# Kernel optimization log

Hardware: AMD Instinct MI355X
Metric: run time of the kernel (lower is better)

Reference implementation:

```python
import jax, jax.numpy as jnp
import numpy as np

S = 7  # output_size
B, C, HF, WF = 8, 256, 160, 160
N = 128
IMG = 640


def setup_inputs() -> dict:
    key = jax.random.key(0)
    k1, k2, k3, k4 = jax.random.split(key, 4)
    feature_map = jax.random.normal(k1, (B, C, HF, WF), jnp.float32)
    # boxes in image-pixel coordinates (the module divides by image_size itself)
    pts = jax.random.uniform(k2, (B, N, 2, 2), jnp.float32, 0.0, float(IMG))
    lo = jnp.min(pts, axis=2)  # (x1, y1)
    hi = jnp.max(pts, axis=2)  # (x2, y2)
    bboxes = jnp.concatenate([lo, hi], axis=-1)  # [B, N, 4]
    proj_w = jax.random.normal(k3, (C, C), jnp.float32) * (1.0 / np.sqrt(C))
    proj_b = jax.random.normal(k4, (C,), jnp.float32) * 0.01
    return {"feature_map": feature_map, "bboxes": bboxes,
            "proj_w": proj_w, "proj_b": proj_b,
            "image_h": IMG, "image_w": IMG}


def _forward(feature_map, bboxes, proj_w, proj_b, image_h, image_w):
    Bb, Cc, Hf, Wf = feature_map.shape
    # 1x1 conv projection
    f = jnp.einsum('bchw,oc->bohw', feature_map, proj_w) + proj_b[None, :, None, None]
    # scale boxes from image coords to feature coords, then integer clip (as in torch code)
    sx = float(Wf) / float(image_w)
    sy = float(Hf) / float(image_h)
    x1 = jnp.clip(jnp.floor(bboxes[..., 0] * sx).astype(jnp.int32), 0, Wf - 1)
    y1 = jnp.clip(jnp.floor(bboxes[..., 1] * sy).astype(jnp.int32), 0, Hf - 1)
    x2 = jnp.clip(jnp.floor(bboxes[..., 2] * sx).astype(jnp.int32), x1 + 1, Wf)
    y2 = jnp.clip(jnp.floor(bboxes[..., 3] * sy).astype(jnp.int32), y1 + 1, Hf)
    Lx = x2 - x1  # [B, N], >= 1 by construction
    Ly = y2 - y1
    i = jnp.arange(S, dtype=jnp.int32)
    # adaptive_avg_pool2d bin edges: start=floor(i*L/S), end=ceil((i+1)*L/S)
    rs = y1[..., None] + (i * Ly[..., None]) // S            # [B, N, S]
    re = y1[..., None] + ((i + 1) * Ly[..., None] + S - 1) // S
    cs = x1[..., None] + (i * Lx[..., None]) // S
    ce = x1[..., None] + ((i + 1) * Lx[..., None] + S - 1) // S
    # summed-area table (zero-padded): I[b,c,y,x] = sum of f[b,c,:y,:x]
    I = jnp.cumsum(jnp.cumsum(f, axis=2), axis=3)
    I = jnp.pad(I, ((0, 0), (0, 0), (1, 0), (1, 0)))

    def per_batch(Ib, rs_b, re_b, cs_b, ce_b):
        # Ib: [C, Hf+1, Wf+1]; index arrays: [N, S]
        tl = Ib[:, rs_b[:, :, None], cs_b[:, None, :]]
        tr = Ib[:, rs_b[:, :, None], ce_b[:, None, :]]
        bl = Ib[:, re_b[:, :, None], cs_b[:, None, :]]
        br = Ib[:, re_b[:, :, None], ce_b[:, None, :]]
        return br - tr - bl + tl  # [C, N, S, S]

    sums = jax.vmap(per_batch)(I, rs, re, cs, ce)  # [B, C, N, S, S]
    counts = ((re - rs)[..., :, None] * (ce - cs)[..., None, :]).astype(f.dtype)  # [B, N, S, S]
    region_features = jnp.transpose(sums, (0, 2, 1, 3, 4)) / counts[:, :, None, :, :]
    # area in raw bbox units, as in the original code
    area_ratios = (bboxes[..., 2] - bboxes[..., 0]) * (bboxes[..., 3] - bboxes[..., 1])
    return region_features, area_ratios


def reference(feature_map, bboxes, proj_w, proj_b, image_h, image_w):
    return _forward(feature_map, bboxes, proj_w, proj_b, image_h, image_w)
```

## Files before the change

kernel.cpp:

```cpp
#include <hip/hip_runtime.h>
#include <hip/hip_bf16.h>

#define BB 8
#define NN 128
#define CC 256
#define HFD 160
#define WFD 160
#define SS 7
#define REGION_OUT_ELEMS (8*128*256*49)

typedef short short8 __attribute__((ext_vector_type(8)));
typedef float f32x4  __attribute__((ext_vector_type(4)));

__global__ __launch_bounds__(256) void k0_convert_w(const float* __restrict__ W,
                                                    __hip_bfloat16* __restrict__ Wb) {
    int o = blockIdx.x;
    int c = threadIdx.x;
    Wb[o * CC + c] = __float2bfloat16(W[o * CC + c]);
}

__global__ __launch_bounds__(256) void k1_rowsum_transpose(const float* __restrict__ fm,
                                                           float* __restrict__ R) {
    int bid = blockIdx.x;
    int cq  = bid & 3;
    int bh  = bid >> 2;
    int h   = bh % HFD;
    int b   = bh / HFD;
    int c0  = cq * 64;
    int t   = threadIdx.x;

    __shared__ float tile[64][161];
    __shared__ float segsum[64][5];

    #pragma unroll
    for (int it = 0; it < 10; ++it) {
        int vid = it * 256 + t;
        int c_l = vid / 40;
        int wq  = vid - c_l * 40;
        f32x4 v = __builtin_nontemporal_load(
            (const f32x4*)(fm + (((size_t)(b * CC + c0 + c_l)) * HFD + h) * WFD + wq * 4));
        tile[c_l][wq * 4 + 0] = v.x;
        tile[c_l][wq * 4 + 1] = v.y;
        tile[c_l][wq * 4 + 2] = v.z;
        tile[c_l][wq * 4 + 3] = v.w;
    }
    __syncthreads();

    int seg = t >> 6;
    int row = t & 63;
    {
        float s = 0.f;
        int w0 = seg * 40;
        #pragma unroll 8
        for (int k = 0; k < 40; ++k) {
            s += tile[row][w0 + k];
            tile[row][w0 + k] = s;
        }
        segsum[row][seg] = s;
    }
    __syncthreads();
    if (t < 64) {
        float a0 = segsum[t][0];
        float a1 = a0 + segsum[t][1];
        float a2 = a1 + segsum[t][2];
        segsum[t][1] = a0;
        segsum[t][2] = a1;
        segsum[t][3] = a2;
    }
    __syncthreads();
    if (seg > 0) {
        float off = segsum[row][seg];
        int w0 = seg * 40;
        #pragma unroll 8
        for (int k = 0; k < 40; ++k) tile[row][w0 + k] += off;
    }
    __syncthreads();

    size_t obase = (((size_t)b * HFD + h) * WFD) * CC + c0;
    #pragma unroll
    for (int it = 0; it < 10; ++it) {
        int vid = it * 256 + t;
        int w   = vid >> 4;
        int cg  = vid & 15;
        float4 o;
        o.x = tile[cg * 4 + 0][w];
        o.y = tile[cg * 4 + 1][w];
        o.z = tile[cg * 4 + 2][w];
        o.w = tile[cg * 4 + 3][w];
        *(float4*)(R + obase + (size_t)w * CC + cg * 4) = o;
    }
}

__global__ __launch_bounds__(256) void k2_colsum(float* __restrict__ I) {
    int w = blockIdx.x % WFD;
    int b = blockIdx.x / WFD;
    int c = threadIdx.x;
    float* p = I + (((size_t)b * HFD) * WFD + w) * CC + c;
    const size_t stride = (size_t)WFD * CC;
    float s = 0.f;
    #pragma unroll 16
    for (int h = 0; h < HFD; ++h) {
        float v = p[(size_t)h * stride];
        s += v;
        p[(size_t)h * stride] = s;
    }
}

#define PB_STRIDE 264

__global__ __launch_bounds__(512) void k3_gather_gemm(
        const float* __restrict__ I, const __hip_bfloat16* __restrict__ Wb,
        const float* __restrict__ bias, const float* __restrict__ bboxes,
        const int* __restrict__ ih_p, const int* __restrict__ iw_p,
        float* __restrict__ out) {
    int bid = blockIdx.x;
    int bn  = ((bid & 7) << 7) | (bid >> 3);
    int b   = bn >> 7;
    int t   = threadIdx.x;
    const int lane = t & 63;
    const int wv   = t >> 6;

    __shared__ __align__(16) __hip_bfloat16 Pb[64 * PB_STRIDE];
    float* stage = (float*)Pb;

    float bx1 = bboxes[bn * 4 + 0];
    float by1 = bboxes[bn * 4 + 1];
    float bx2 = bboxes[bn * 4 + 2];
    float by2 = bboxes[bn * 4 + 3];
    float sx = (float)WFD / (float)iw_p[0];
    float sy = (float)HFD / (float)ih_p[0];

    int x1 = min(max((int)floorf(bx1 * sx), 0), WFD - 1);
    int y1 = min(max((int)floorf(by1 * sy), 0), HFD - 1);
    int x2 = min(max((int)floorf(bx2 * sx), x1 + 1), WFD);
    int y2 = min(max((int)floorf(by2 * sy), y1 + 1), HFD);
    int Lx = x2 - x1, Ly = y2 - y1;

    {
        const float* Ibl = I + (size_t)b * HFD * WFD * CC + 4 * lane;
        unsigned short* pbs = (unsigned short*)Pb;

#define GATHER_CELL(cellv)                                                       \
        {                                                                        \
            int cell = (cellv);                                                  \
            int i_ = cell / SS, j_ = cell % SS;                                  \
            int rs_ = y1 + (i_ * Ly) / SS;                                       \
            int re_ = y1 + ((i_ + 1) * Ly + SS - 1) / SS;                        \
            int cs_ = x1 + (j_ * Lx) / SS;                                       \
            int ce_ = x1 + ((j_ + 1) * Lx + SS - 1) / SS;                        \
            int r1 = re_ - 1;                                                    \
            int r0 = max(rs_ - 1, 0);                                            \
            int c1 = ce_ - 1;                                                    \
            int c0 = max(cs_ - 1, 0);                                            \
            float rm = (rs_ > 0) ? 1.f : 0.f;                                    \
            float cm = (cs_ > 0) ? 1.f : 0.f;                                    \
            f32x4 br = *(const f32x4*)(Ibl + ((size_t)(r1 * WFD + c1)) * CC);    \
            f32x4 tr = *(const f32x4*)(Ibl + ((size_t)(r0 * WFD + c1)) * CC);    \
            f32x4 bl = *(const f32x4*)(Ibl + ((size_t)(r1 * WFD + c0)) * CC);    \
            f32x4 tl = *(const f32x4*)(Ibl + ((size_t)(r0 * WFD + c0)) * CC);    \
            f32x4 s = (br - tr * rm) - (bl - tl * rm) * cm;                      \
            float inv = 1.f / ((float)(re_ - rs_) * (float)(ce_ - cs_));         \
            ushort4 pk;                                                          \
            {                                                                    \
                __hip_bfloat16 h0 = __float2bfloat16(s.x * inv);                 \
                __hip_bfloat16 h1 = __float2bfloat16(s.y * inv);                 \
                __hip_bfloat16 h2 = __float2bfloat16(s.z * inv);                 \
                __hip_bfloat16 h3 = __float2bfloat16(s.w * inv);                 \
                pk.x = *(unsigned short*)&h0;                                    \
                pk.y = *(unsigned short*)&h1;                                    \
                pk.z = *(unsigned short*)&h2;                                    \
                pk.w = *(unsigned short*)&h3;                                    \
            }                                                                    \
            *(ushort4*)(pbs + cell * PB_STRIDE + 4 * lane) = pk;                 \
        }

        #pragma unroll
        for (int k = 0; k < 6; ++k) GATHER_CELL(wv * 6 + k);
        if (wv == 0) GATHER_CELL(48);
#undef GATHER_CELL
    }
    __syncthreads();

    const int ln   = lane & 15;
    const int quad = lane >> 4;
    const int ob0  = wv * 32;

    f32x4 z = {0.f, 0.f, 0.f, 0.f};
    f32x4 acc[2][4];
    #pragma unroll
    for (int mt = 0; mt < 2; ++mt)
        #pragma unroll
        for (int nt = 0; nt < 4; ++nt) acc[mt][nt] = z;

    {
        const short* A = (const short*)Wb;
        #pragma unroll
        for (int k0 = 0; k0 < CC; k0 += 32) {
            short8 a[2], bf[4];
            #pragma unroll
            for (int mt = 0; mt < 2; ++mt)
                a[mt] = *(const short8*)(A + (ob0 + mt * 16 + ln) * CC + k0 + quad * 8);
            #pragma unroll
            for (int nt = 0; nt < 4; ++nt)
                bf[nt] = *(const short8*)((const short*)Pb + (nt * 16 + ln) * PB_STRIDE + k0 + quad * 8);
            #pragma unroll
            for (int mt = 0; mt < 2; ++mt)
                #pragma unroll
                for (int nt = 0; nt < 4; ++nt)
                    acc[mt][nt] = __builtin_amdgcn_mfma_f32_16x16x32_bf16(a[mt], bf[nt], acc[mt][nt], 0, 0, 0);
        }
    }

    size_t obase = (size_t)bn * CC * 49;
    #pragma unroll
    for (int half = 0; half < 2; ++half) {
        __syncthreads();
        if ((wv >> 2) == half) {
            int ob0l = (wv & 3) * 32;
            #pragma unroll
            for (int mt = 0; mt < 2; ++mt) {
                f32x4 bv = *(const f32x4*)(bias + ob0 + mt * 16 + quad * 4);
                #pragma unroll
                for (int nt = 0; nt < 4; ++nt) {
                    int cell = nt * 16 + ln;
                    if (cell < 49) {
                        #pragma unroll
                        for (int reg = 0; reg < 4; ++reg) {
                            int ol = ob0l + mt * 16 + quad * 4 + reg;
                            stage[ol * 49 + cell] = acc[mt][nt][reg] + bv[reg];
                        }
                    }
                }
            }
        }
        __syncthreads();
        const f32x4* sv = (const f32x4*)stage;
        float* gbase = out + obase + (size_t)half * (128 * 49);
        for (int i = t; i < (128 * 49) / 4; i += 512) {
            __builtin_nontemporal_store(sv[i], (f32x4*)(gbase + 4 * i));
        }
    }

    if (t == 0) {
        __builtin_nontemporal_store((bx2 - bx1) * (by2 - by1), &out[REGION_OUT_ELEMS + bn]);
    }
}

extern "C" void kernel_launch(void* const* d_in, const int* in_sizes, int n_in,
                              void* d_out, int out_size, void* d_ws, size_t ws_size,
                              hipStream_t stream) {
    const float* fm     = (const float*)d_in[0];
    const float* bboxes = (const float*)d_in[1];
    const float* W      = (const float*)d_in[2];
    const float* bias   = (const float*)d_in[3];
    const int*   ih     = (const int*)d_in[4];
    const int*   iw     = (const int*)d_in[5];
    float* out = (float*)d_out;

    __hip_bfloat16* Wb = (__hip_bfloat16*)d_ws;
    float* I = (float*)((char*)d_ws + (size_t)CC * CC * 2 + 256);
    I = (float*)(((uintptr_t)I + 1023) & ~(uintptr_t)1023);

    k0_convert_w<<<CC, 256, 0, stream>>>(W, Wb);
    k1_rowsum_transpose<<<BB * HFD * 4, 256, 0, stream>>>(fm, I);
    k2_colsum<<<BB * WFD, 256, 0, stream>>>(I);
    k3_gather_gemm<<<BB * NN, 512, 0, stream>>>(I, Wb, bias, bboxes, ih, iw, out);
}
```

Measured before the change: 411.0 us.

## Fuse column prefix into row-scan kernel with per-block offsets

The row-scan kernel now processes 8 consecutive rows per block and keeps a running column sum in registers, so it writes a blockwise-inclusive integral image in one pass. The separate full read-modify-write column-sum pass over the 210MB table is replaced by a small kernel that only computes per-block row offsets. The gather kernel adds these offsets at lookup time, which doubles its gather loads (eight instead of four per cell). It also gets a launch_bounds occupancy hint. The block grid shrinks to 640 blocks, which may reduce parallelism during the scan.

```diff
diff --git a/kernel.cpp b/kernel.cpp
--- a/kernel.cpp
+++ b/kernel.cpp
@@ -7,6 +7,8 @@
 #define HFD 160
 #define WFD 160
 #define SS 7
+#define HB 8
+#define NHB (HFD / HB)
 #define REGION_OUT_ELEMS (8*128*256*49)
 
 typedef short short8 __attribute__((ext_vector_type(8)));
@@ -19,97 +21,106 @@
     Wb[o * CC + c] = __float2bfloat16(W[o * CC + c]);
 }
 
-__global__ __launch_bounds__(256) void k1_rowsum_transpose(const float* __restrict__ fm,
-                                                           float* __restrict__ R) {
+__global__ __launch_bounds__(256) void k1_rowscan_block(const float* __restrict__ fm,
+                                                        float* __restrict__ Ip) {
     int bid = blockIdx.x;
-    int cq  = bid & 3;
-    int bh  = bid >> 2;
-    int h   = bh % HFD;
-    int b   = bh / HFD;
+    int hb  = bid % NHB;
+    int cq  = (bid / NHB) & 3;
+    int b   = bid / (NHB * 4);
     int c0  = cq * 64;
     int t   = threadIdx.x;
 
     __shared__ float tile[64][161];
     __shared__ float segsum[64][5];
 
-    #pragma unroll
-    for (int it = 0; it < 10; ++it) {
-        int vid = it * 256 + t;
-        int c_l = vid / 40;
-        int wq  = vid - c_l * 40;
-        f32x4 v = __builtin_nontemporal_load(
-            (const f32x4*)(fm + (((size_t)(b * CC + c0 + c_l)) * HFD + h) * WFD + wq * 4));
-        tile[c_l][wq * 4 + 0] = v.x;
-        tile[c_l][wq * 4 + 1] = v.y;
-        tile[c_l][wq * 4 + 2] = v.z;
-        tile[c_l][wq * 4 + 3] = v.w;
-    }
-    __syncthreads();
-
     int seg = t >> 6;
     int row = t & 63;
-    {
-        float s = 0.f;
-        int w0 = seg * 40;
-        #pragma unroll 8
-        for (int k = 0; k < 40; ++k) {
-            s += tile[row][w0 + k];
-            tile[row][w0 + k] = s;
-        }
-        segsum[row][seg] = s;
-    }
-    __syncthreads();
-    if (t < 64) {
-        float a0 = segsum[t][0];
-        float a1 = a0 + segsum[t][1];
-        float a2 = a1 + segsum[t][2];
-        segsum[t][1] = a0;
-        segsum[t][2] = a1;
-        segsum[t][3] = a2;
-    }
-    __syncthreads();
-    if (seg > 0) {
-        float off = segsum[row][seg];
-        int w0 = seg * 40;
-        #pragma unroll 8
-        for (int k = 0; k < 40; ++k) tile[row][w0 + k] += off;
-    }
-    __syncthreads();
-
-    size_t obase = (((size_t)b * HFD + h) * WFD) * CC + c0;
-    #pragma unroll
-    for (int it = 0; it < 10; ++it) {
-        int vid = it * 256 + t;
-        int w   = vid >> 4;
-        int cg  = vid & 15;
-        float4 o;
-        o.x = tile[cg * 4 + 0][w];
-        o.y = tile[cg * 4 + 1][w];
-        o.z = tile[cg * 4 + 2][w];
-        o.w = tile[cg * 4 + 3][w];
-        *(float4*)(R + obase + (size_t)w * CC + cg * 4) = o;
-    }
-}
-
-__global__ __launch_bounds__(256) void k2_colsum(float* __restrict__ I) {
+
+    f32x4 csum[10];
+    #pragma unroll
+    for (int it = 0; it < 10; ++it) csum[it] = (f32x4){0.f, 0.f, 0.f, 0.f};
+
+    for (int hh = 0; hh < HB; ++hh) {
+        int h = hb * HB + hh;
+        __syncthreads();
+
+        #pragma unroll
+        for (int it = 0; it < 10; ++it) {
+            int vid = it * 256 + t;
+            int c_l = vid / 40;
+            int wq  = vid - c_l * 40;
+            f32x4 v = __builtin_nontemporal_load(
+                (const f32x4*)(fm + (((size_t)(b * CC + c0 + c_l)) * HFD + h) * WFD + wq * 4));
+            tile[c_l][wq * 4 + 0] = v.x;
+            tile[c_l][wq * 4 + 1] = v.y;
+            tile[c_l][wq * 4 + 2] = v.z;
+            tile[c_l][wq * 4 + 3] = v.w;
+        }
+        __syncthreads();
+
+        {
+            float s = 0.f;
+            int w0 = seg * 40;
+            #pragma unroll 8
+            for (int k = 0; k < 40; ++k) {
+                s += tile[row][w0 + k];
+                tile[row][w0 + k] = s;
+            }
+            segsum[row][seg] = s;
+        }
+        __syncthreads();
+        if (t < 64) {
+            float a0 = segsum[t][0];
+            float a1 = a0 + segsum[t][1];
+            float a2 = a1 + segsum[t][2];
+            segsum[t][1] = a0;
+            segsum[t][2] = a1;
+            segsum[t][3] = a2;
+        }
+        __syncthreads();
+        if (seg > 0) {
+            float off = segsum[row][seg];
+            int w0 = seg * 40;
+            #pragma unroll 8
+            for (int k = 0; k < 40; ++k) tile[row][w0 + k] += off;
+        }
+        __syncthreads();
+
+        size_t obase = (((size_t)b * HFD + h) * WFD) * CC + c0;
+        #pragma unroll
+        for (int it = 0; it < 10; ++it) {
+            int vid = it * 256 + t;
+            int w   = vid >> 4;
+            int cg  = vid & 15;
+            f32x4 cur;
+            cur.x = tile[cg * 4 + 0][w];
+            cur.y = tile[cg * 4 + 1][w];
+            cur.z = tile[cg * 4 + 2][w];
+            cur.w = tile[cg * 4 + 3][w];
+            csum[it] += cur;
+            *(f32x4*)(Ip + obase + (size_t)w * CC + cg * 4) = csum[it];
+        }
+    }
+}
+
+__global__ __launch_bounds__(256) void k2_offsets(const float* __restrict__ Ip,
+                                                  float* __restrict__ O) {
     int w = blockIdx.x % WFD;
     int b = blockIdx.x / WFD;
     int c = threadIdx.x;
-    float* p = I + (((size_t)b * HFD) * WFD + w) * CC + c;
-    const size_t stride = (size_t)WFD * CC;
-    float s = 0.f;
-    #pragma unroll 16
-    for (int h = 0; h < HFD; ++h) {
-        float v = p[(size_t)h * stride];
-        s += v;
-        p[(size_t)h * stride] = s;
+    float run = 0.f;
+    #pragma unroll
+    for (int hb = 0; hb < NHB; ++hb) {
+        O[(((size_t)b * NHB + hb) * WFD + w) * CC + c] = run;
+        run += Ip[(((size_t)b * HFD + (hb * HB + HB - 1)) * WFD + w) * CC + c];
     }
 }
 
 #define PB_STRIDE 264
 
-__global__ __launch_bounds__(512) void k3_gather_gemm(
-        const float* __restrict__ I, const __hip_bfloat16* __restrict__ Wb,
+__global__ __launch_bounds__(512, 4) void k3_gather_gemm(
+        const float* __restrict__ Ip, const float* __restrict__ O,
+        const __hip_bfloat16* __restrict__ Wb,
         const float* __restrict__ bias, const float* __restrict__ bboxes,
         const int* __restrict__ ih_p, const int* __restrict__ iw_p,
         float* __restrict__ out) {
@@ -137,7 +148,8 @@
     int Lx = x2 - x1, Ly = y2 - y1;
 
     {
-        const float* Ibl = I + (size_t)b * HFD * WFD * CC + 4 * lane;
+        const float* Ibl = Ip + (size_t)b * HFD * WFD * CC + 4 * lane;
+        const float* Obl = O + (size_t)b * NHB * WFD * CC + 4 * lane;
         unsigned short* pbs = (unsigned short*)Pb;
 
 #define GATHER_CELL(cellv)                                                       \
@@ -152,12 +164,17 @@
             int r0 = max(rs_ - 1, 0);                                            \
             int c1 = ce_ - 1;                                                    \
             int c0 = max(cs_ - 1, 0);                                            \
+            int hb1 = r1 >> 3, hb0 = r0 >> 3;                                    \
             float rm = (rs_ > 0) ? 1.f : 0.f;                                    \
             float cm = (cs_ > 0) ? 1.f : 0.f;                                    \
-            f32x4 br = *(const f32x4*)(Ibl + ((size_t)(r1 * WFD + c1)) * CC);    \
-            f32x4 tr = *(const f32x4*)(Ibl + ((size_t)(r0 * WFD + c1)) * CC);    \
-            f32x4 bl = *(const f32x4*)(Ibl + ((size_t)(r1 * WFD + c0)) * CC);    \
-            f32x4 tl = *(const f32x4*)(Ibl + ((size_t)(r0 * WFD + c0)) * CC);    \
+            f32x4 br = *(const f32x4*)(Ibl + ((size_t)(r1 * WFD + c1)) * CC)     \
+                     + *(const f32x4*)(Obl + ((size_t)(hb1 * WFD + c1)) * CC);   \
+            f32x4 tr = *(const f32x4*)(Ibl + ((size_t)(r0 * WFD + c1)) * CC)     \
+                     + *(const f32x4*)(Obl + ((size_t)(hb0 * WFD + c1)) * CC);   \
+            f32x4 bl = *(const f32x4*)(Ibl + ((size_t)(r1 * WFD + c0)) * CC)     \
+                     + *(const f32x4*)(Obl + ((size_t)(hb1 * WFD + c0)) * CC);   \
+            f32x4 tl = *(const f32x4*)(Ibl + ((size_t)(r0 * WFD + c0)) * CC)     \
+                     + *(const f32x4*)(Obl + ((size_t)(hb0 * WFD + c0)) * CC);   \
             f32x4 s = (br - tr * rm) - (bl - tl * rm) * cm;                      \
             float inv = 1.f / ((float)(re_ - rs_) * (float)(ce_ - cs_));         \
             ushort4 pk;                                                          \
@@ -258,11 +275,13 @@
     float* out = (float*)d_out;
 
     __hip_bfloat16* Wb = (__hip_bfloat16*)d_ws;
-    float* I = (float*)((char*)d_ws + (size_t)CC * CC * 2 + 256);
-    I = (float*)(((uintptr_t)I + 1023) & ~(uintptr_t)1023);
+    float* Ip = (float*)((char*)d_ws + (size_t)CC * CC * 2 + 256);
+    Ip = (float*)(((uintptr_t)Ip + 1023) & ~(uintptr_t)1023);
+    float* O = (float*)((char*)Ip + (size_t)BB * HFD * WFD * CC * 4);
+    O = (float*)(((uintptr_t)O + 1023) & ~(uintptr_t)1023);
 
     k0_convert_w<<<CC, 256, 0, stream>>>(W, Wb);
-    k1_rowsum_transpose<<<BB * HFD * 4, 256, 0, stream>>>(fm, I);
-    k2_colsum<<<BB * WFD, 256, 0, stream>>>(I);
-    k3_gather_gemm<<<BB * NN, 512, 0, stream>>>(I, Wb, bias, bboxes, ih, iw, out);
-}
+    k1_rowscan_block<<<BB * 4 * NHB, 256, 0, stream>>>(fm, Ip);
+    k2_offsets<<<BB * WFD, 256, 0, stream>>>(Ip, O);
+    k3_gather_gemm<<<BB * NN, 512, 0, stream>>>(Ip, O, Wb, bias, bboxes, ih, iw, out);
+}
```

Result: faster. 396.0 us (-3.7%).
